# Kernel tuning notes

Measured on AMD Instinct MI355X. Metric: run time of the kernel, lower is better.

The kernel has to match this reference:

```python
import jax, jax.numpy as jnp
import numpy as np

DIM = 768
N_HEADS = 12
HEAD_DIM = DIM // N_HEADS
MAX_REL = 3  # hardcoded in the module


def setup_inputs() -> dict:
    key = jax.random.key(0)
    ks = jax.random.split(key, 10)
    B, L = 4, 1024
    def xavier(k, shape):
        fan_in, fan_out = shape[-2], shape[-1]
        a = jnp.sqrt(6.0 / (fan_in + fan_out))
        return jax.random.uniform(k, shape, jnp.float32, -a, a)
    return {
        "query": jax.random.normal(ks[0], (B, L, DIM), jnp.float32),
        "key":   jax.random.normal(ks[1], (B, L, DIM), jnp.float32),
        "value": jax.random.normal(ks[2], (B, L, DIM), jnp.float32),
        "Wq": xavier(ks[3], (DIM, DIM)),
        "Wk": xavier(ks[4], (DIM, DIM)),
        "Wv": xavier(ks[5], (DIM, DIM)),
        "Wproj": xavier(ks[6], (DIM, DIM)),
        "b_proj": jnp.zeros((DIM,), jnp.float32),
        "rel_k_table": xavier(ks[7], (2 * MAX_REL + 1, HEAD_DIM)),
        "rel_v_table": xavier(ks[8], (2 * MAX_REL + 1, HEAD_DIM)),
    }


def _rel_embed(table, len_q, len_k):
    # [len_q, len_k, head_dim] gathered from clipped relative distances
    dist = jnp.arange(len_k)[None, :] - jnp.arange(len_q)[:, None]
    idx = jnp.clip(dist, -MAX_REL, MAX_REL) + MAX_REL
    return table[idx]


def reference(query, key, value, Wq, Wk, Wv, Wproj, b_proj, rel_k_table, rel_v_table):
    B, Lq, _ = query.shape
    Lk = key.shape[1]
    H, hd = N_HEADS, HEAD_DIM
    scale = hd ** (-0.5)

    q = query @ Wq.T                      # [B, Lq, D]
    k = key @ Wk.T                        # [B, Lk, D]
    v = value @ Wv.T                      # [B, Lk, D]

    qh = q.reshape(B, Lq, H, hd).transpose(0, 2, 1, 3)   # [B,H,Lq,hd]
    kh = k.reshape(B, Lk, H, hd).transpose(0, 2, 1, 3)
    vh = v.reshape(B, Lk, H, hd).transpose(0, 2, 1, 3)

    # content-content scores
    attn1 = jnp.einsum('bhqd,bhkd->bhqk', qh, kh)
    # content-relative-position scores
    rk = _rel_embed(rel_k_table, Lq, Lk)                  # [Lq,Lk,hd]
    attn2 = jnp.einsum('bhqd,qkd->bhqk', qh, rk)
    # NOTE: original code DIVIDES by scale (= hd**-0.5), i.e. multiplies by sqrt(hd)
    attn = (attn1 + attn2) / scale
    attn = jax.nn.softmax(attn, axis=-1)                  # [B,H,Lq,Lk]

    w1 = jnp.einsum('bhqk,bhkd->bhqd', attn, vh)
    rv = _rel_embed(rel_v_table, Lq, Lk)                  # [Lq,Lk,hd]
    w2 = jnp.einsum('bhqk,qkd->bhqd', attn, rv)

    x = (w1 + w2).transpose(0, 2, 1, 3).reshape(B, Lq, H * hd)
    x = x @ Wproj.T + b_proj
    return (x, attn)
```

## Files before the change

### kernel.cpp

```cpp
#include <hip/hip_runtime.h>

#define DIMM 768
#define NH 12
#define HD 64
#define LSEQ 1024
#define BATCH 4
#define NXE 3145728
#define NWE 589824

typedef __bf16 bf16x8 __attribute__((ext_vector_type(8)));
typedef float f32x4 __attribute__((ext_vector_type(4)));
typedef unsigned short u16;
typedef unsigned short u16x8 __attribute__((ext_vector_type(8)));

static __device__ __forceinline__ u16 f2bf(float f) {
  unsigned u = __builtin_bit_cast(unsigned, f);
  u += 0x7fffu + ((u >> 16) & 1u);
  return (u16)(u >> 16);
}
static __device__ __forceinline__ float bf2f(u16 h) {
  unsigned u = ((unsigned)h) << 16;
  return __builtin_bit_cast(float, u);
}
static __device__ __forceinline__ bf16x8 ld8bf(const u16* p) {
  uint4 u = *(const uint4*)p;
  return __builtin_bit_cast(bf16x8, u);
}
#define MFMA(a, b, c) __builtin_amdgcn_mfma_f32_16x16x32_bf16(a, b, c, 0, 0, 0)
#define GLL(g, s)                                                      \
  __builtin_amdgcn_global_load_lds(                                    \
      (const __attribute__((address_space(1))) void*)(g),              \
      (__attribute__((address_space(3))) void*)(s), 16, 0, 0)

__global__ __launch_bounds__(256) void convert(
    const float* __restrict__ q_in, const float* __restrict__ k_in,
    const float* __restrict__ v_in, const float* __restrict__ Wq,
    const float* __restrict__ Wk, const float* __restrict__ Wv,
    const float* __restrict__ Wp, u16* __restrict__ AqH, u16* __restrict__ AqL,
    u16* __restrict__ AkH, u16* __restrict__ AkL, u16* __restrict__ Av,
    u16* __restrict__ WqH, u16* __restrict__ WqL, u16* __restrict__ WkH,
    u16* __restrict__ WkL, u16* __restrict__ Wvr, u16* __restrict__ Wpr) {
  long i = ((long)blockIdx.x * 256 + threadIdx.x) * 4;
  const float* src;
  u16 *dh, *dl = nullptr;
  long off;
  if (i < NXE) { src = q_in; dh = AqH; dl = AqL; off = i; }
  else if (i < 2L * NXE) { src = k_in; dh = AkH; dl = AkL; off = i - NXE; }
  else if (i < 3L * NXE) { src = v_in; dh = Av; off = i - 2L * NXE; }
  else {
    long j = i - 3L * NXE;
    int which = (int)(j / NWE);
    off = j % NWE;
    if (which == 0) { src = Wq; dh = WqH; dl = WqL; }
    else if (which == 1) { src = Wk; dh = WkH; dl = WkL; }
    else if (which == 2) { src = Wv; dh = Wvr; }
    else { src = Wp; dh = Wpr; }
  }
  float4 v = *(const float4*)(src + off);
  ushort4 h;
  h.x = f2bf(v.x); h.y = f2bf(v.y); h.z = f2bf(v.z); h.w = f2bf(v.w);
  *(ushort4*)(dh + off) = h;
  if (dl) {
    ushort4 lo;
    lo.x = f2bf(v.x - bf2f(h.x)); lo.y = f2bf(v.y - bf2f(h.y));
    lo.z = f2bf(v.z - bf2f(h.z)); lo.w = f2bf(v.w - bf2f(h.w));
    *(ushort4*)(dl + off) = lo;
  }
}

__global__ __launch_bounds__(256) void gemm_multi(
    int mode0, const u16* __restrict__ AqH, const u16* __restrict__ AqL,
    const u16* __restrict__ AkH, const u16* __restrict__ AkL,
    const u16* __restrict__ Av, const u16* __restrict__ WqH,
    const u16* __restrict__ WqL, const u16* __restrict__ WkH,
    const u16* __restrict__ WkL, const u16* __restrict__ Wvr,
    const u16* __restrict__ Wpr, const u16* __restrict__ wbuf,
    u16* __restrict__ qhi, u16* __restrict__ qlo, u16* __restrict__ khi,
    u16* __restrict__ klo, u16* __restrict__ vT, float* __restrict__ outp,
    const float* __restrict__ bias) {
  __shared__ u16 sAh[64 * 32], sAl[64 * 32];
  __shared__ u16 sBh[128 * 32], sBl[128 * 32];
  const int mode = mode0 + blockIdx.z;
  const u16 *Ah, *Al = nullptr, *Bh, *Bl = nullptr;
  if (mode == 0) { Ah = AqH; Al = AqL; Bh = WqH; Bl = WqL; }
  else if (mode == 1) { Ah = AkH; Al = AkL; Bh = WkH; Bl = WkL; }
  else if (mode == 2) { Ah = Av; Bh = Wvr; }
  else { Ah = wbuf; Bh = Wpr; }
  const int t = threadIdx.x, w = t >> 6, l = t & 63;
  const int quad = l >> 4, l15 = l & 15;
  const int m0 = blockIdx.x * 64, n0 = blockIdx.y * 128;
  const int wm = (w >> 1) * 32, wn = (w & 1) * 64;
  const int srow = t >> 2, scol = (t & 3) * 8;
  const u16* gA = Ah + (m0 + srow) * DIMM + scol;
  const u16* gB = Bh + (n0 + srow) * DIMM + scol;
  u16* lA = sAh + w * 512;
  u16* lB = sBh + w * 512;
  f32x4 acc[2][4] = {};
  if (mode < 2) {
    const u16* gAl = Al + (m0 + srow) * DIMM + scol;
    const u16* gBl = Bl + (n0 + srow) * DIMM + scol;
    u16* lAl = sAl + w * 512;
    u16* lBl = sBl + w * 512;
    for (int k0 = 0; k0 < DIMM; k0 += 32) {
      GLL(gA + k0, lA);
      GLL(gAl + k0, lAl);
      GLL(gB + k0, lB);
      GLL(gB + 64 * DIMM + k0, lB + 2048);
      GLL(gBl + k0, lBl);
      GLL(gBl + 64 * DIMM + k0, lBl + 2048);
      __syncthreads();
      bf16x8 ah[2], aL[2], bh[4], bL[4];
#pragma unroll
      for (int i = 0; i < 2; ++i) {
        int r = (wm + i * 16 + l15) * 32 + quad * 8;
        ah[i] = __builtin_bit_cast(bf16x8, *(const uint4*)(sAh + r));
        aL[i] = __builtin_bit_cast(bf16x8, *(const uint4*)(sAl + r));
      }
#pragma unroll
      for (int j = 0; j < 4; ++j) {
        int r = (wn + j * 16 + l15) * 32 + quad * 8;
        bh[j] = __builtin_bit_cast(bf16x8, *(const uint4*)(sBh + r));
        bL[j] = __builtin_bit_cast(bf16x8, *(const uint4*)(sBl + r));
      }
#pragma unroll
      for (int i = 0; i < 2; ++i)
#pragma unroll
        for (int j = 0; j < 4; ++j) {
          acc[i][j] = MFMA(ah[i], bh[j], acc[i][j]);
          acc[i][j] = MFMA(ah[i], bL[j], acc[i][j]);
          acc[i][j] = MFMA(aL[i], bh[j], acc[i][j]);
        }
      __syncthreads();
    }
  } else {
    for (int k0 = 0; k0 < DIMM; k0 += 32) {
      GLL(gA + k0, lA);
      GLL(gB + k0, lB);
      GLL(gB + 64 * DIMM + k0, lB + 2048);
      __syncthreads();
      bf16x8 ah[2], bh[4];
#pragma unroll
      for (int i = 0; i < 2; ++i)
        ah[i] = __builtin_bit_cast(
            bf16x8, *(const uint4*)(sAh + (wm + i * 16 + l15) * 32 + quad * 8));
#pragma unroll
      for (int j = 0; j < 4; ++j)
        bh[j] = __builtin_bit_cast(
            bf16x8, *(const uint4*)(sBh + (wn + j * 16 + l15) * 32 + quad * 8));
#pragma unroll
      for (int i = 0; i < 2; ++i)
#pragma unroll
        for (int j = 0; j < 4; ++j) acc[i][j] = MFMA(ah[i], bh[j], acc[i][j]);
      __syncthreads();
    }
  }
  u16* oh = (mode == 0) ? qhi : khi;
  u16* ol = (mode == 0) ? qlo : klo;
#pragma unroll
  for (int i = 0; i < 2; ++i)
#pragma unroll
    for (int j = 0; j < 4; ++j)
#pragma unroll
      for (int r = 0; r < 4; ++r) {
        int grow = m0 + wm + i * 16 + quad * 4 + r;
        int gcol = n0 + wn + j * 16 + l15;
        float c = acc[i][j][r];
        int b = grow >> 10, ll = grow & 1023, h = gcol >> 6, d = gcol & 63;
        if (mode < 2) {
          int idx = ((b * NH + h) * LSEQ + ll) * HD + d;
          u16 hi = f2bf(c);
          oh[idx] = hi;
          ol[idx] = f2bf(c - bf2f(hi));
        } else if (mode == 2) {
          vT[((b * NH + h) * HD + d) * LSEQ + ll] = f2bf(c);
        } else {
          outp[grow * DIMM + gcol] = c + bias[gcol];
        }
      }
}

__global__ __launch_bounds__(256) void attn_core(
    const u16* __restrict__ qhi, const u16* __restrict__ qlo,
    const u16* __restrict__ khi, const u16* __restrict__ klo,
    const u16* __restrict__ vT, const float* __restrict__ relk,
    const float* __restrict__ relv, float* __restrict__ attn_out,
    u16* __restrict__ wbuf) {
  __shared__ __align__(16) float S[16][1028];
  __shared__ float qrel[16][7];
  __shared__ float arel[16][7];
  __shared__ float rvt[7][64];

  const int qt = blockIdx.x, h = blockIdx.y, b = blockIdx.z;
  const int q0 = qt * 16;
  const int tid = threadIdx.x, wave = tid >> 6, lane = tid & 63;
  const int quad = lane >> 4, l15 = lane & 15;
  const int bhd = b * NH + h;

  for (int t = tid; t < 7 * HD; t += 256) rvt[t >> 6][t & 63] = relv[t];
  if (tid < 112) {
    int q = tid / 7, rr = tid % 7;
    const u16* qp = qhi + (bhd * LSEQ + q0 + q) * HD;
    const u16* lp = qlo + (bhd * LSEQ + q0 + q) * HD;
    const float* tp = relk + rr * HD;
    float s = 0.f;
    for (int d = 0; d < HD; ++d) s += (bf2f(qp[d]) + bf2f(lp[d])) * tp[d];
    qrel[q][rr] = s;
  }

  {
    const int qbase = (bhd * LSEQ + q0 + l15) * HD + quad * 8;
    bf16x8 ah0 = ld8bf(qhi + qbase);
    bf16x8 ah1 = ld8bf(qhi + qbase + 32);
    bf16x8 al0 = ld8bf(qlo + qbase);
    bf16x8 al1 = ld8bf(qlo + qbase + 32);
    const u16* bh = khi + (bhd * LSEQ + wave * 16 + l15) * HD + quad * 8;
    const u16* bl = klo + (bhd * LSEQ + wave * 16 + l15) * HD + quad * 8;
    bf16x8 kh0 = ld8bf(bh), kh1 = ld8bf(bh + 32);
    bf16x8 kl0 = ld8bf(bl), kl1 = ld8bf(bl + 32);
    for (int it = 0; it < 16; ++it) {
      bf16x8 nh0 = kh0, nh1 = kh1, nl0 = kl0, nl1 = kl1;
      if (it < 15) {
        const u16* ph = bh + (it + 1) * 4096;
        const u16* pl = bl + (it + 1) * 4096;
        nh0 = ld8bf(ph); nh1 = ld8bf(ph + 32);
        nl0 = ld8bf(pl); nl1 = ld8bf(pl + 32);
      }
      f32x4 acc = {};
      acc = MFMA(ah0, kh0, acc);
      acc = MFMA(ah1, kh1, acc);
      acc = MFMA(ah0, kl0, acc);
      acc = MFMA(ah1, kl1, acc);
      acc = MFMA(al0, kh0, acc);
      acc = MFMA(al1, kh1, acc);
      const int nt = wave + it * 4;
#pragma unroll
      for (int r = 0; r < 4; ++r) S[quad * 4 + r][nt * 16 + l15] = acc[r];
      kh0 = nh0; kh1 = nh1; kl0 = nl0; kl1 = nl1;
    }
  }
  __syncthreads();

  for (int rr = 0; rr < 4; ++rr) {
    const int qr = wave * 4 + rr;
    const int qa = q0 + qr;
    float vals[16];
    float mx = -3.4e38f;
#pragma unroll
    for (int i = 0; i < 16; ++i) {
      int c = i * 64 + lane;
      int d = c - qa;
      int ri = d < -3 ? 0 : (d > 3 ? 6 : d + 3);
      float s = (S[qr][c] + qrel[qr][ri]) * 8.0f;
      vals[i] = s;
      mx = fmaxf(mx, s);
    }
#pragma unroll
    for (int off = 32; off > 0; off >>= 1) mx = fmaxf(mx, __shfl_xor(mx, off));
    float sum = 0.f, s0 = 0.f, s6 = 0.f;
#pragma unroll
    for (int i = 0; i < 16; ++i) {
      int c = i * 64 + lane;
      float e = __expf(vals[i] - mx);
      vals[i] = e;
      sum += e;
      if (c <= qa - 3) s0 += e;
      if (c >= qa + 3) s6 += e;
    }
#pragma unroll
    for (int off = 32; off > 0; off >>= 1) {
      sum += __shfl_xor(sum, off);
      s0 += __shfl_xor(s0, off);
      s6 += __shfl_xor(s6, off);
    }
    float rn = 1.0f / sum;
    float* ao = attn_out + ((size_t)(bhd * LSEQ + qa)) * LSEQ;
#pragma unroll
    for (int i = 0; i < 16; ++i) {
      int c = i * 64 + lane;
      float p = vals[i] * rn;
      S[qr][c] = p;
      ao[c] = p;
    }
    if (lane == 0) { arel[qr][0] = s0 * rn; arel[qr][6] = s6 * rn; }
  }
  __syncthreads();
  if (tid < 80) {
    int qr = tid / 5, m = tid % 5;
    int kidx = q0 + qr + m - 2;
    arel[qr][m + 1] = (kidx >= 0 && kidx < LSEQ) ? S[qr][kidx] : 0.f;
  }
  __syncthreads();

  {
    const u16* vb = vT + (bhd * HD + wave * 16 + l15) * LSEQ;
    f32x4 acc = {};
    for (int kk = 0; kk < LSEQ; kk += 32) {
      int ak = kk + quad * 8;
      float4 p0 = *(const float4*)&S[l15][ak];
      float4 p1 = *(const float4*)&S[l15][ak + 4];
      u16x8 up;
      up[0] = f2bf(p0.x); up[1] = f2bf(p0.y); up[2] = f2bf(p0.z); up[3] = f2bf(p0.w);
      up[4] = f2bf(p1.x); up[5] = f2bf(p1.y); up[6] = f2bf(p1.z); up[7] = f2bf(p1.w);
      bf16x8 aP = __builtin_bit_cast(bf16x8, up);
      bf16x8 bV = ld8bf(vb + ak);
      acc = MFMA(aP, bV, acc);
    }
    const int col = wave * 16 + l15;
#pragma unroll
    for (int r = 0; r < 4; ++r) {
      int row = quad * 4 + r;
      float w2 = 0.f;
#pragma unroll
      for (int t = 0; t < 7; ++t) w2 += arel[row][t] * rvt[t][col];
      wbuf[(b * LSEQ + q0 + row) * DIMM + h * HD + col] = f2bf(acc[r] + w2);
    }
  }
}

extern "C" void kernel_launch(void* const* d_in, const int* in_sizes, int n_in,
                              void* d_out, int out_size, void* d_ws, size_t ws_size,
                              hipStream_t stream) {
  const float* q_in = (const float*)d_in[0];
  const float* k_in = (const float*)d_in[1];
  const float* v_in = (const float*)d_in[2];
  const float* Wq = (const float*)d_in[3];
  const float* Wk = (const float*)d_in[4];
  const float* Wv = (const float*)d_in[5];
  const float* Wp = (const float*)d_in[6];
  const float* bias = (const float*)d_in[7];
  const float* relk = (const float*)d_in[8];
  const float* relv = (const float*)d_in[9];
  float* out = (float*)d_out;

  u16* p = (u16*)d_ws;
  u16 *AqH = p, *AqL = AqH + NXE, *AkH = AqL + NXE, *AkL = AkH + NXE,
      *Av = AkL + NXE;
  u16 *WqH = Av + NXE, *WqL = WqH + NWE, *WkH = WqL + NWE, *WkL = WkH + NWE,
      *Wvr = WkL + NWE, *Wpr = Wvr + NWE;
  u16 *qhi = Wpr + NWE, *qlo = qhi + NXE, *khi = qlo + NXE, *klo = khi + NXE,
      *vT = klo + NXE, *wbuf = vT + NXE;

  convert<<<(3 * NXE + 4 * NWE) / 1024, 256, 0, stream>>>(
      q_in, k_in, v_in, Wq, Wk, Wv, Wp, AqH, AqL, AkH, AkL, Av, WqH, WqL, WkH,
      WkL, Wvr, Wpr);
  gemm_multi<<<dim3(64, 6, 3), 256, 0, stream>>>(
      0, AqH, AqL, AkH, AkL, Av, WqH, WqL, WkH, WkL, Wvr, Wpr, wbuf, qhi, qlo,
      khi, klo, vT, out, bias);
  attn_core<<<dim3(64, NH, BATCH), 256, 0, stream>>>(
      qhi, qlo, khi, klo, vT, relk, relv, out + NXE, wbuf);
  gemm_multi<<<dim3(64, 6, 1), 256, 0, stream>>>(
      3, AqH, AqL, AkH, AkL, Av, WqH, WqL, WkH, WkL, Wvr, Wpr, wbuf, qhi, qlo,
      khi, klo, vT, out, bias);
}
```

Measured before the change: 487.9 us.

## Enlarge GEMM tiles to 128x128 and keep attention scores in registers

```diff
diff --git a/kernel.cpp b/kernel.cpp
--- a/kernel.cpp
+++ b/kernel.cpp
@@ -11,7 +11,6 @@
 typedef __bf16 bf16x8 __attribute__((ext_vector_type(8)));
 typedef float f32x4 __attribute__((ext_vector_type(4)));
 typedef unsigned short u16;
-typedef unsigned short u16x8 __attribute__((ext_vector_type(8)));
 
 static __device__ __forceinline__ u16 f2bf(float f) {
   unsigned u = __builtin_bit_cast(unsigned, f);
@@ -68,7 +67,7 @@
   }
 }
 
-__global__ __launch_bounds__(256) void gemm_multi(
+__global__ __launch_bounds__(256, 3) void gemm_multi(
     int mode0, const u16* __restrict__ AqH, const u16* __restrict__ AqL,
     const u16* __restrict__ AkH, const u16* __restrict__ AkL,
     const u16* __restrict__ Av, const u16* __restrict__ WqH,
@@ -78,7 +77,7 @@
     u16* __restrict__ qhi, u16* __restrict__ qlo, u16* __restrict__ khi,
     u16* __restrict__ klo, u16* __restrict__ vT, float* __restrict__ outp,
     const float* __restrict__ bias) {
-  __shared__ u16 sAh[64 * 32], sAl[64 * 32];
+  __shared__ u16 sAh[128 * 32], sAl[128 * 32];
   __shared__ u16 sBh[128 * 32], sBl[128 * 32];
   const int mode = mode0 + blockIdx.z;
   const u16 *Ah, *Al = nullptr, *Bh, *Bl = nullptr;
@@ -88,14 +87,14 @@
   else { Ah = wbuf; Bh = Wpr; }
   const int t = threadIdx.x, w = t >> 6, l = t & 63;
   const int quad = l >> 4, l15 = l & 15;
-  const int m0 = blockIdx.x * 64, n0 = blockIdx.y * 128;
-  const int wm = (w >> 1) * 32, wn = (w & 1) * 64;
+  const int m0 = blockIdx.x * 128, n0 = blockIdx.y * 128;
+  const int wm = (w >> 1) * 64, wn = (w & 1) * 64;
   const int srow = t >> 2, scol = (t & 3) * 8;
   const u16* gA = Ah + (m0 + srow) * DIMM + scol;
   const u16* gB = Bh + (n0 + srow) * DIMM + scol;
   u16* lA = sAh + w * 512;
   u16* lB = sBh + w * 512;
-  f32x4 acc[2][4] = {};
+  f32x4 acc[4][4] = {};
   if (mode < 2) {
     const u16* gAl = Al + (m0 + srow) * DIMM + scol;
     const u16* gBl = Bl + (n0 + srow) * DIMM + scol;
@@ -103,44 +102,55 @@
     u16* lBl = sBl + w * 512;
     for (int k0 = 0; k0 < DIMM; k0 += 32) {
       GLL(gA + k0, lA);
+      GLL(gA + 64 * DIMM + k0, lA + 2048);
       GLL(gAl + k0, lAl);
+      GLL(gAl + 64 * DIMM + k0, lAl + 2048);
       GLL(gB + k0, lB);
       GLL(gB + 64 * DIMM + k0, lB + 2048);
       GLL(gBl + k0, lBl);
       GLL(gBl + 64 * DIMM + k0, lBl + 2048);
       __syncthreads();
-      bf16x8 ah[2], aL[2], bh[4], bL[4];
-#pragma unroll
-      for (int i = 0; i < 2; ++i) {
-        int r = (wm + i * 16 + l15) * 32 + quad * 8;
-        ah[i] = __builtin_bit_cast(bf16x8, *(const uint4*)(sAh + r));
-        aL[i] = __builtin_bit_cast(bf16x8, *(const uint4*)(sAl + r));
-      }
-#pragma unroll
-      for (int j = 0; j < 4; ++j) {
-        int r = (wn + j * 16 + l15) * 32 + quad * 8;
-        bh[j] = __builtin_bit_cast(bf16x8, *(const uint4*)(sBh + r));
-        bL[j] = __builtin_bit_cast(bf16x8, *(const uint4*)(sBl + r));
-      }
-#pragma unroll
-      for (int i = 0; i < 2; ++i)
-#pragma unroll
-        for (int j = 0; j < 4; ++j) {
-          acc[i][j] = MFMA(ah[i], bh[j], acc[i][j]);
-          acc[i][j] = MFMA(ah[i], bL[j], acc[i][j]);
-          acc[i][j] = MFMA(aL[i], bh[j], acc[i][j]);
-        }
+      bf16x8 ah[4], bh[4], xl[4];
+#pragma unroll
+      for (int i = 0; i < 4; ++i)
+        ah[i] = __builtin_bit_cast(
+            bf16x8, *(const uint4*)(sAh + (wm + i * 16 + l15) * 32 + quad * 8));
+#pragma unroll
+      for (int j = 0; j < 4; ++j)
+        bh[j] = __builtin_bit_cast(
+            bf16x8, *(const uint4*)(sBh + (wn + j * 16 + l15) * 32 + quad * 8));
+#pragma unroll
+      for (int i = 0; i < 4; ++i)
+#pragma unroll
+        for (int j = 0; j < 4; ++j) acc[i][j] = MFMA(ah[i], bh[j], acc[i][j]);
+#pragma unroll
+      for (int i = 0; i < 4; ++i)
+        xl[i] = __builtin_bit_cast(
+            bf16x8, *(const uint4*)(sAl + (wm + i * 16 + l15) * 32 + quad * 8));
+#pragma unroll
+      for (int i = 0; i < 4; ++i)
+#pragma unroll
+        for (int j = 0; j < 4; ++j) acc[i][j] = MFMA(xl[i], bh[j], acc[i][j]);
+#pragma unroll
+      for (int j = 0; j < 4; ++j)
+        xl[j] = __builtin_bit_cast(
+            bf16x8, *(const uint4*)(sBl + (wn + j * 16 + l15) * 32 + quad * 8));
+#pragma unroll
+      for (int i = 0; i < 4; ++i)
+#pragma unroll
+        for (int j = 0; j < 4; ++j) acc[i][j] = MFMA(ah[i], xl[j], acc[i][j]);
       __syncthreads();
     }
   } else {
     for (int k0 = 0; k0 < DIMM; k0 += 32) {
       GLL(gA + k0, lA);
+      GLL(gA + 64 * DIMM + k0, lA + 2048);
       GLL(gB + k0, lB);
       GLL(gB + 64 * DIMM + k0, lB + 2048);
       __syncthreads();
-      bf16x8 ah[2], bh[4];
-#pragma unroll
-      for (int i = 0; i < 2; ++i)
+      bf16x8 ah[4], bh[4];
+#pragma unroll
+      for (int i = 0; i < 4; ++i)
         ah[i] = __builtin_bit_cast(
             bf16x8, *(const uint4*)(sAh + (wm + i * 16 + l15) * 32 + quad * 8));
 #pragma unroll
@@ -148,7 +158,7 @@
         bh[j] = __builtin_bit_cast(
             bf16x8, *(const uint4*)(sBh + (wn + j * 16 + l15) * 32 + quad * 8));
 #pragma unroll
-      for (int i = 0; i < 2; ++i)
+      for (int i = 0; i < 4; ++i)
 #pragma unroll
         for (int j = 0; j < 4; ++j) acc[i][j] = MFMA(ah[i], bh[j], acc[i][j]);
       __syncthreads();
@@ -157,7 +167,7 @@
   u16* oh = (mode == 0) ? qhi : khi;
   u16* ol = (mode == 0) ? qlo : klo;
 #pragma unroll
-  for (int i = 0; i < 2; ++i)
+  for (int i = 0; i < 4; ++i)
 #pragma unroll
     for (int j = 0; j < 4; ++j)
 #pragma unroll
@@ -179,16 +189,17 @@
       }
 }
 
-__global__ __launch_bounds__(256) void attn_core(
+__global__ __launch_bounds__(256, 3) void attn_core(
     const u16* __restrict__ qhi, const u16* __restrict__ qlo,
     const u16* __restrict__ khi, const u16* __restrict__ klo,
     const u16* __restrict__ vT, const float* __restrict__ relk,
     const float* __restrict__ relv, float* __restrict__ attn_out,
     u16* __restrict__ wbuf) {
-  __shared__ __align__(16) float S[16][1028];
+  __shared__ __align__(16) u16 Pb[16][1032];
   __shared__ float qrel[16][7];
   __shared__ float arel[16][7];
   __shared__ float rvt[7][64];
+  __shared__ float red[4][16][4];
 
   const int qt = blockIdx.x, h = blockIdx.y, b = blockIdx.z;
   const int q0 = qt * 16;
@@ -205,8 +216,11 @@
     float s = 0.f;
     for (int d = 0; d < HD; ++d) s += (bf2f(qp[d]) + bf2f(lp[d])) * tp[d];
     qrel[q][rr] = s;
-  }
-
+    arel[q][rr] = 0.f;
+  }
+  __syncthreads();
+
+  f32x4 sc[16];
   {
     const int qbase = (bhd * LSEQ + q0 + l15) * HD + quad * 8;
     bf16x8 ah0 = ld8bf(qhi + qbase);
@@ -217,6 +231,7 @@
     const u16* bl = klo + (bhd * LSEQ + wave * 16 + l15) * HD + quad * 8;
     bf16x8 kh0 = ld8bf(bh), kh1 = ld8bf(bh + 32);
     bf16x8 kl0 = ld8bf(bl), kl1 = ld8bf(bl + 32);
+#pragma unroll
     for (int it = 0; it < 16; ++it) {
       bf16x8 nh0 = kh0, nh1 = kh1, nl0 = kl0, nl1 = kl1;
       if (it < 15) {
@@ -232,62 +247,98 @@
       acc = MFMA(ah1, kl1, acc);
       acc = MFMA(al0, kh0, acc);
       acc = MFMA(al1, kh1, acc);
-      const int nt = wave + it * 4;
-#pragma unroll
-      for (int r = 0; r < 4; ++r) S[quad * 4 + r][nt * 16 + l15] = acc[r];
+      sc[it] = acc;
       kh0 = nh0; kh1 = nh1; kl0 = nl0; kl1 = nl1;
     }
   }
+
+  const int colbase = wave * 16 + l15;
+  const int dbase = colbase - q0 - quad * 4;
+  float mrow[4] = {-3.4e38f, -3.4e38f, -3.4e38f, -3.4e38f};
+#pragma unroll
+  for (int it = 0; it < 16; ++it)
+#pragma unroll
+    for (int r = 0; r < 4; ++r) {
+      int d = dbase + it * 64 - r;
+      int ri = d < -3 ? 0 : (d > 3 ? 6 : d + 3);
+      float s = (sc[it][r] + qrel[quad * 4 + r][ri]) * 8.0f;
+      sc[it][r] = s;
+      mrow[r] = fmaxf(mrow[r], s);
+    }
+#pragma unroll
+  for (int m = 1; m <= 8; m <<= 1)
+#pragma unroll
+    for (int r = 0; r < 4; ++r) mrow[r] = fmaxf(mrow[r], __shfl_xor(mrow[r], m));
+  if (l15 < 4) {
+    float mv = l15 == 0 ? mrow[0] : l15 == 1 ? mrow[1] : l15 == 2 ? mrow[2] : mrow[3];
+    red[0][quad * 4 + l15][wave] = mv;
+  }
   __syncthreads();
-
-  for (int rr = 0; rr < 4; ++rr) {
-    const int qr = wave * 4 + rr;
-    const int qa = q0 + qr;
-    float vals[16];
-    float mx = -3.4e38f;
-#pragma unroll
-    for (int i = 0; i < 16; ++i) {
-      int c = i * 64 + lane;
-      int d = c - qa;
-      int ri = d < -3 ? 0 : (d > 3 ? 6 : d + 3);
-      float s = (S[qr][c] + qrel[qr][ri]) * 8.0f;
-      vals[i] = s;
-      mx = fmaxf(mx, s);
-    }
-#pragma unroll
-    for (int off = 32; off > 0; off >>= 1) mx = fmaxf(mx, __shfl_xor(mx, off));
-    float sum = 0.f, s0 = 0.f, s6 = 0.f;
-#pragma unroll
-    for (int i = 0; i < 16; ++i) {
-      int c = i * 64 + lane;
-      float e = __expf(vals[i] - mx);
-      vals[i] = e;
-      sum += e;
-      if (c <= qa - 3) s0 += e;
-      if (c >= qa + 3) s6 += e;
-    }
-#pragma unroll
-    for (int off = 32; off > 0; off >>= 1) {
-      sum += __shfl_xor(sum, off);
-      s0 += __shfl_xor(s0, off);
-      s6 += __shfl_xor(s6, off);
-    }
-    float rn = 1.0f / sum;
-    float* ao = attn_out + ((size_t)(bhd * LSEQ + qa)) * LSEQ;
-#pragma unroll
-    for (int i = 0; i < 16; ++i) {
-      int c = i * 64 + lane;
-      float p = vals[i] * rn;
-      S[qr][c] = p;
-      ao[c] = p;
-    }
-    if (lane == 0) { arel[qr][0] = s0 * rn; arel[qr][6] = s6 * rn; }
+  float mx[4];
+#pragma unroll
+  for (int r = 0; r < 4; ++r) {
+    int row = quad * 4 + r;
+    mx[r] = fmaxf(fmaxf(red[0][row][0], red[0][row][1]),
+                  fmaxf(red[0][row][2], red[0][row][3]));
+  }
+
+  float sum[4] = {}, s0a[4] = {}, s6a[4] = {};
+#pragma unroll
+  for (int it = 0; it < 16; ++it)
+#pragma unroll
+    for (int r = 0; r < 4; ++r) {
+      float e = __expf(sc[it][r] - mx[r]);
+      sc[it][r] = e;
+      int d = dbase + it * 64 - r;
+      sum[r] += e;
+      if (d <= -3) s0a[r] += e;
+      if (d >= 3) s6a[r] += e;
+    }
+#pragma unroll
+  for (int m = 1; m <= 8; m <<= 1)
+#pragma unroll
+    for (int r = 0; r < 4; ++r) {
+      sum[r] += __shfl_xor(sum[r], m);
+      s0a[r] += __shfl_xor(s0a[r], m);
+      s6a[r] += __shfl_xor(s6a[r], m);
+    }
+  if (l15 < 4) {
+    int row = quad * 4 + l15;
+    float sv = l15 == 0 ? sum[0] : l15 == 1 ? sum[1] : l15 == 2 ? sum[2] : sum[3];
+    float a0 = l15 == 0 ? s0a[0] : l15 == 1 ? s0a[1] : l15 == 2 ? s0a[2] : s0a[3];
+    float a6 = l15 == 0 ? s6a[0] : l15 == 1 ? s6a[1] : l15 == 2 ? s6a[2] : s6a[3];
+    red[1][row][wave] = sv;
+    red[2][row][wave] = a0;
+    red[3][row][wave] = a6;
   }
   __syncthreads();
-  if (tid < 80) {
-    int qr = tid / 5, m = tid % 5;
-    int kidx = q0 + qr + m - 2;
-    arel[qr][m + 1] = (kidx >= 0 && kidx < LSEQ) ? S[qr][kidx] : 0.f;
+  float rn[4];
+#pragma unroll
+  for (int r = 0; r < 4; ++r) {
+    int row = quad * 4 + r;
+    float s = red[1][row][0] + red[1][row][1] + red[1][row][2] + red[1][row][3];
+    rn[r] = 1.0f / s;
+    if (wave == 0 && l15 == 0) {
+      float t0 = red[2][row][0] + red[2][row][1] + red[2][row][2] + red[2][row][3];
+      float t6 = red[3][row][0] + red[3][row][1] + red[3][row][2] + red[3][row][3];
+      arel[row][0] = t0 * rn[r];
+      arel[row][6] = t6 * rn[r];
+    }
+  }
+
+  float* aob = attn_out + ((size_t)(bhd * LSEQ + q0)) * LSEQ;
+#pragma unroll
+  for (int it = 0; it < 16; ++it) {
+    int col = colbase + it * 64;
+#pragma unroll
+    for (int r = 0; r < 4; ++r) {
+      int row = quad * 4 + r;
+      float p = sc[it][r] * rn[r];
+      aob[row * LSEQ + col] = p;
+      Pb[row][col] = f2bf(p);
+      int d = dbase + it * 64 - r;
+      if (d >= -2 && d <= 2) arel[row][d + 3] = p;
+    }
   }
   __syncthreads();
 
@@ -296,12 +347,7 @@
     f32x4 acc = {};
     for (int kk = 0; kk < LSEQ; kk += 32) {
       int ak = kk + quad * 8;
-      float4 p0 = *(const float4*)&S[l15][ak];
-      float4 p1 = *(const float4*)&S[l15][ak + 4];
-      u16x8 up;
-      up[0] = f2bf(p0.x); up[1] = f2bf(p0.y); up[2] = f2bf(p0.z); up[3] = f2bf(p0.w);
-      up[4] = f2bf(p1.x); up[5] = f2bf(p1.y); up[6] = f2bf(p1.z); up[7] = f2bf(p1.w);
-      bf16x8 aP = __builtin_bit_cast(bf16x8, up);
+      bf16x8 aP = __builtin_bit_cast(bf16x8, *(const uint4*)&Pb[l15][ak]);
       bf16x8 bV = ld8bf(vb + ak);
       acc = MFMA(aP, bV, acc);
     }
@@ -343,12 +389,12 @@
   convert<<<(3 * NXE + 4 * NWE) / 1024, 256, 0, stream>>>(
       q_in, k_in, v_in, Wq, Wk, Wv, Wp, AqH, AqL, AkH, AkL, Av, WqH, WqL, WkH,
       WkL, Wvr, Wpr);
-  gemm_multi<<<dim3(64, 6, 3), 256, 0, stream>>>(
+  gemm_multi<<<dim3(32, 6, 3), 256, 0, stream>>>(
       0, AqH, AqL, AkH, AkL, Av, WqH, WqL, WkH, WkL, Wvr, Wpr, wbuf, qhi, qlo,
       khi, klo, vT, out, bias);
   attn_core<<<dim3(64, NH, BATCH), 256, 0, stream>>>(
       qhi, qlo, khi, klo, vT, relk, relv, out + NXE, wbuf);
-  gemm_multi<<<dim3(64, 6, 1), 256, 0, stream>>>(
+  gemm_multi<<<dim3(32, 6, 1), 256, 0, stream>>>(
       3, AqH, AqL, AkH, AkL, Av, WqH, WqL, WkH, WkL, Wvr, Wpr, wbuf, qhi, qlo,
       khi, klo, vT, out, bias);
 }
```

Measured after the change: 467.4 us. 4.2% less time.
